# Optimization experiments

Hardware: AMD Instinct MI355X
Metric: run time of the kernel (lower is better)

## Reference

```python
import jax, jax.numpy as jnp
import numpy as np

B, T, E = 2, 2048, 1024
H = 16
DH = E // H  # 64
DFF = 4 * E
EPS = 1e-5


def _layernorm(x, gamma, beta):
    mu = jnp.mean(x, axis=-1, keepdims=True)
    var = jnp.mean((x - mu) ** 2, axis=-1, keepdims=True)
    return (x - mu) * jax.lax.rsqrt(var + EPS) * gamma + beta


def setup_inputs() -> dict:
    key = jax.random.key(0)
    ks = jax.random.split(key, 16)
    s_e = 1.0 / np.sqrt(E)
    s_f = 1.0 / np.sqrt(DFF)
    return {
        "x": jax.random.normal(ks[0], (B, T, E), jnp.float32),
        # per-head QKV projections, stacked over heads [H, E, DH]
        "Wq": jax.random.normal(ks[1], (H, E, DH), jnp.float32) * s_e,
        "bq": jnp.zeros((H, DH), jnp.float32),
        "Wk": jax.random.normal(ks[2], (H, E, DH), jnp.float32) * s_e,
        "bk": jnp.zeros((H, DH), jnp.float32),
        "Wv": jax.random.normal(ks[3], (H, E, DH), jnp.float32) * s_e,
        "bv": jnp.zeros((H, DH), jnp.float32),
        # output projection
        "Wo": jax.random.normal(ks[4], (E, E), jnp.float32) * s_e,
        "bo": jnp.zeros((E,), jnp.float32),
        # feed-forward
        "W1": jax.random.normal(ks[5], (E, DFF), jnp.float32) * s_e,
        "b1": jnp.zeros((DFF,), jnp.float32),
        "W2": jax.random.normal(ks[6], (DFF, E), jnp.float32) * s_f,
        "b2": jnp.zeros((E,), jnp.float32),
        # layernorms
        "gamma1": jnp.ones((E,), jnp.float32),
        "beta1": jnp.zeros((E,), jnp.float32),
        "gamma2": jnp.ones((E,), jnp.float32),
        "beta2": jnp.zeros((E,), jnp.float32),
    }


def reference(x, Wq, bq, Wk, bk, Wv, bv, Wo, bo, W1, b1, W2, b2,
              gamma1, beta1, gamma2, beta2):
    Bc, Tc, Ec = x.shape
    # --- multi-head causal self-attention (dropout = eval/identity) ---
    xn = _layernorm(x, gamma1, beta1)
    q = jnp.einsum('bte,hed->bhtd', xn, Wq) + bq[:, None, :]
    k = jnp.einsum('bte,hed->bhtd', xn, Wk) + bk[:, None, :]
    v = jnp.einsum('bte,hed->bhtd', xn, Wv) + bv[:, None, :]
    scale = 1.0 / np.sqrt(q.shape[-1])
    scores = jnp.einsum('bhtd,bhsd->bhts', q, k) * scale  # [B,H,T,T]
    causal = jnp.tril(jnp.ones((Tc, Tc), bool))
    scores = jnp.where(causal, scores, jnp.float32(-1e9))
    attn = jax.nn.softmax(scores, axis=-1)
    out = jnp.einsum('bhts,bhsd->bhtd', attn, v)          # [B,H,T,DH]
    out = out.transpose(0, 2, 1, 3).reshape(Bc, Tc, Ec)    # concat heads
    out = out @ Wo + bo
    x = x + out
    # --- feed-forward ---
    xn2 = _layernorm(x, gamma2, beta2)
    h = jax.nn.relu(xn2 @ W1 + b1)
    x = x + (h @ W2 + b2)
    return x
```

## Files before the change

### kernel.cpp

```cpp
#include <hip/hip_runtime.h>
#include <stdint.h>

#define BT    4096
#define EDIM  1024
#define TLEN  2048
#define NH    16
#define DHH   64
#define DFFN  4096

typedef short short8 __attribute__((ext_vector_type(8)));
typedef float f32x4  __attribute__((ext_vector_type(4)));

typedef const __attribute__((address_space(1))) unsigned int* gas_ptr;
typedef __attribute__((address_space(3))) unsigned int*       las_ptr;

__device__ __forceinline__ float bf2f(unsigned short u) {
    union { unsigned int i; float f; } c; c.i = ((unsigned int)u) << 16; return c.f;
}
__device__ __forceinline__ unsigned short f2bf(float f) {
    union { float f; unsigned int i; } c; c.f = f;
    unsigned int u = c.i;
    unsigned int r = u + 0x7fffu + ((u >> 16) & 1u);
    return (unsigned short)(r >> 16);
}
__device__ __forceinline__ float fexp2(float x) {
#if __has_builtin(__builtin_amdgcn_exp2f)
    return __builtin_amdgcn_exp2f(x);
#else
    return __expf(x * 0.69314718056f);
#endif
}
__device__ __forceinline__ void gload16(const unsigned short* g, unsigned short* l) {
    __builtin_amdgcn_global_load_lds((gas_ptr)g, (las_ptr)l, 16, 0, 0);
}

template<int QKV>
__global__ __launch_bounds__(256) void transpose_kernel(
    const float* src, unsigned short* dst, int Kdim, int srcStride)
{
    __shared__ float T[64][65];
    int t = threadIdx.x;
    int n0 = blockIdx.x * 64, k0 = blockIdx.y * 64;
    int r = t >> 4, c4 = (t & 15) * 4;
    #pragma unroll
    for (int i = 0; i < 4; i++) {
        int rr = r + i * 16;
        const float* p;
        if (QKV) p = src + ((size_t)(n0 >> 6)) * 65536 + (size_t)(k0 + rr) * 64 + c4;
        else     p = src + (size_t)(k0 + rr) * srcStride + n0 + c4;
        float4 v = *(const float4*)p;
        T[c4 + 0][rr] = v.x;
        T[c4 + 1][rr] = v.y;
        T[c4 + 2][rr] = v.z;
        T[c4 + 3][rr] = v.w;
    }
    __syncthreads();
    int rn = t >> 2, ck = (t & 3) * 16;
    short8 o0, o1;
    #pragma unroll
    for (int j = 0; j < 8; j++) o0[j] = (short)f2bf(T[rn][ck + j]);
    #pragma unroll
    for (int j = 0; j < 8; j++) o1[j] = (short)f2bf(T[rn][ck + 8 + j]);
    unsigned short* dp = dst + (size_t)(n0 + rn) * Kdim + k0 + ck;
    *(short8*)dp       = o0;
    *(short8*)(dp + 8) = o1;
}

__global__ __launch_bounds__(256) void vtrans_kernel(
    const unsigned short* __restrict__ v, unsigned short* __restrict__ vt)
{
    __shared__ __align__(16) unsigned short T[64][72];
    int bh = blockIdx.x, st = blockIdx.y;
    int t = threadIdx.x;
    int r = t >> 2, c = (t & 3) * 16;
    const unsigned short* src = v + ((size_t)bh * TLEN + st * 64) * DHH;
    short8 a0 = *(const short8*)(src + r * DHH + c);
    short8 a1 = *(const short8*)(src + r * DHH + c + 8);
    *(short8*)&T[r][c]     = a0;
    *(short8*)&T[r][c + 8] = a1;
    __syncthreads();
    int d = t >> 2;
    short8 o0, o1;
    #pragma unroll
    for (int j = 0; j < 8; j++) o0[j] = (short)T[c + j][d];
    #pragma unroll
    for (int j = 0; j < 8; j++) o1[j] = (short)T[c + 8 + j][d];
    unsigned short* dst = vt + ((size_t)bh * DHH + d) * TLEN + st * 64 + c;
    *(short8*)dst       = o0;
    *(short8*)(dst + 8) = o1;
}

__global__ __launch_bounds__(256) void bias_fuse_kernel(
    const float* __restrict__ bq, const float* __restrict__ bk,
    const float* __restrict__ bv, float* __restrict__ dst)
{
    int t = blockIdx.x * 256 + threadIdx.x;
    const float* src = (t < 1024) ? bq : (t < 2048) ? bk : bv;
    dst[t] = src[t & 1023];
}

template<int F32IN>
__global__ __launch_bounds__(256) void ln_stats_kernel(
    const void* __restrict__ x, float* __restrict__ mu_out, float* __restrict__ rstd_out)
{
    int row = blockIdx.x, tid = threadIdx.x;
    size_t off = (size_t)row * EDIM + tid * 4;
    float v0, v1, v2, v3;
    if (F32IN) {
        float4 a = *(const float4*)((const float*)x + off);
        v0 = a.x; v1 = a.y; v2 = a.z; v3 = a.w;
    } else {
        ushort4 raw = *(const ushort4*)((const unsigned short*)x + off);
        v0 = bf2f(raw.x); v1 = bf2f(raw.y); v2 = bf2f(raw.z); v3 = bf2f(raw.w);
    }
    float s  = v0 + v1 + v2 + v3;
    float ss = v0*v0 + v1*v1 + v2*v2 + v3*v3;
    #pragma unroll
    for (int o = 1; o < 64; o <<= 1) {
        s  += __shfl_xor(s,  o, 64);
        ss += __shfl_xor(ss, o, 64);
    }
    __shared__ float red[8];
    int wave = tid >> 6;
    if ((tid & 63) == 0) { red[wave*2] = s; red[wave*2+1] = ss; }
    __syncthreads();
    if (tid == 0) {
        s  = red[0] + red[2] + red[4] + red[6];
        ss = red[1] + red[3] + red[5] + red[7];
        float mu  = s * (1.0f / EDIM);
        float var = ss * (1.0f / EDIM) - mu * mu;
        mu_out[row]   = mu;
        rstd_out[row] = rsqrtf(var + 1e-5f);
    }
}

template<int F32IN>
__global__ __launch_bounds__(256) void ln_apply_kernel(
    const void* __restrict__ x, const float* __restrict__ mu, const float* __restrict__ rstd,
    const float* __restrict__ g, const float* __restrict__ b, unsigned short* __restrict__ out)
{
    int row = blockIdx.x, tid = threadIdx.x;
    float m = mu[row], rs = rstd[row];
    size_t off = (size_t)row * EDIM + tid * 4;
    float v0, v1, v2, v3;
    if (F32IN) {
        float4 a = *(const float4*)((const float*)x + off);
        v0 = a.x; v1 = a.y; v2 = a.z; v3 = a.w;
    } else {
        ushort4 raw = *(const ushort4*)((const unsigned short*)x + off);
        v0 = bf2f(raw.x); v1 = bf2f(raw.y); v2 = bf2f(raw.z); v3 = bf2f(raw.w);
    }
    float4 gv = *(const float4*)(g + tid * 4);
    float4 bv = *(const float4*)(b + tid * 4);
    ushort4 o;
    o.x = f2bf((v0 - m) * rs * gv.x + bv.x);
    o.y = f2bf((v1 - m) * rs * gv.y + bv.y);
    o.z = f2bf((v2 - m) * rs * gv.z + bv.z);
    o.w = f2bf((v3 - m) * rs * gv.w + bv.w);
    *(ushort4*)(out + off) = o;
}

#define V_QKV  0
#define V_WO   1
#define V_FF1  2
#define V_FF2A 3
#define V_FF2B 4

template<int VARIANT, int BN>
__global__ __launch_bounds__(256) void gemm_bt_kernel(
    const unsigned short* A,
    const unsigned short* Bt,
    const float* bias,
    const void* resid,
    void* out,
    int N, int K)
{
    constexpr int NJ = BN / 32;
    __shared__ __align__(16) unsigned short As[128 * 64];
    __shared__ __align__(16) unsigned short Bs[BN * 64];
    int tid  = threadIdx.x;
    int lane = tid & 63, wave = tid >> 6;
    int quad = lane >> 4, l16 = lane & 15;
    int wr = wave >> 1, wc = wave & 1;
    int m0 = blockIdx.y * 128, n0 = blockIdx.x * BN;

    f32x4 acc[4][NJ];
    #pragma unroll
    for (int i = 0; i < 4; i++)
        #pragma unroll
        for (int j = 0; j < NJ; j++) acc[i][j] = (f32x4){0.f, 0.f, 0.f, 0.f};

    int lr = lane >> 3;
    int lc = (lane & 7) * 8;

    for (int k0 = 0; k0 < K; k0 += 64) {
        #pragma unroll
        for (int i = 0; i < 4; i++) {
            int r = (i * 4 + wave) * 8 + lr;
            gload16(A + (size_t)(m0 + r) * K + k0 + lc, &As[(i * 4 + wave) * 512]);
        }
        #pragma unroll
        for (int i = 0; i < NJ; i++) {
            int r = (i * 4 + wave) * 8 + lr;
            gload16(Bt + (size_t)(n0 + r) * K + k0 + lc, &Bs[(i * 4 + wave) * 512]);
        }
        __syncthreads();

        #pragma unroll
        for (int ks = 0; ks < 2; ks++) {
            short8 af[4], bf[NJ];
            #pragma unroll
            for (int i = 0; i < 4; i++)
                af[i] = *(const short8*)(&As[(wr * 64 + i * 16 + l16) * 64 + ks * 32 + quad * 8]);
            #pragma unroll
            for (int j = 0; j < NJ; j++)
                bf[j] = *(const short8*)(&Bs[(wc * (BN / 2) + j * 16 + l16) * 64 + ks * 32 + quad * 8]);
            #pragma unroll
            for (int i = 0; i < 4; i++)
                #pragma unroll
                for (int j = 0; j < NJ; j++)
                    acc[i][j] = __builtin_amdgcn_mfma_f32_16x16x32_bf16(af[i], bf[j], acc[i][j], 0, 0, 0);
        }

        __syncthreads();
    }

    #pragma unroll
    for (int j = 0; j < NJ; j++) {
        int c = n0 + wc * (BN / 2) + j * 16 + l16;
        float bi = (VARIANT == V_FF2A) ? 0.0f : bias[c];
        #pragma unroll
        for (int i = 0; i < 4; i++) {
            #pragma unroll
            for (int r = 0; r < 4; r++) {
                int m = m0 + wr * 64 + i * 16 + quad * 4 + r;
                float val = acc[i][j][r] + bi;
                if (VARIANT == V_WO)
                    val += ((const float*)resid)[(size_t)m * N + c];
                if (VARIANT == V_FF2B)
                    val += bf2f(((const unsigned short*)resid)[(size_t)m * N + c])
                         + ((const float*)out)[(size_t)m * N + c];
                if (VARIANT == V_FF1)
                    val = fmaxf(val, 0.0f);
                if (VARIANT == V_QKV) {
                    int b = m >> 11, t = m & 2047;
                    int mat = c >> 10, cc = c & 1023;
                    int h = cc >> 6, d = cc & 63;
                    ((unsigned short*)out)[(size_t)mat * 4194304 +
                        (((size_t)(b * NH + h)) * TLEN + t) * DHH + d] = f2bf(val);
                } else if (VARIANT == V_FF2A || VARIANT == V_FF2B) {
                    ((float*)out)[(size_t)m * N + c] = val;
                } else {
                    ((unsigned short*)out)[(size_t)m * N + c] = f2bf(val);
                }
            }
        }
    }
}

__global__ __launch_bounds__(256) void attn_kernel(
    const unsigned short* __restrict__ q,
    const unsigned short* __restrict__ k,
    const unsigned short* __restrict__ vt,
    unsigned short* __restrict__ att)
{
    __shared__ __align__(16) unsigned short Ks[128 * 72];
    __shared__ __align__(16) unsigned short Vs[64 * 136];
    __shared__ __align__(16) unsigned short Ps[4][16 * 136];
    int tid  = threadIdx.x;
    int lane = tid & 63, wave = tid >> 6;
    int quad = lane >> 4, l16 = lane & 15;

    int flat = blockIdx.x;
    int xcd  = flat & 7, idx = flat >> 3;
    int bh   = xcd * 4 + (idx >> 5);
    int qt   = 31 - (idx & 31);
    int q0   = qt * 64;
    int qw   = q0 + wave * 16;

    const unsigned short* Qb = q  + ((size_t)bh * TLEN + qw) * DHH;
    const unsigned short* Kb = k  + (size_t)bh * TLEN * DHH;
    const unsigned short* Vb = vt + (size_t)bh * DHH * TLEN;

    short8 aq0 = *(const short8*)(Qb + l16 * DHH + quad * 8);
    short8 aq1 = *(const short8*)(Qb + l16 * DHH + 32 + quad * 8);

    f32x4 o[4];
    #pragma unroll
    for (int n = 0; n < 4; n++) o[n] = (f32x4){0.f, 0.f, 0.f, 0.f};
    f32x4 mrow = {-1e30f, -1e30f, -1e30f, -1e30f};
    f32x4 lrow = {0.f, 0.f, 0.f, 0.f};
    unsigned short* Pw = Ps[wave];
    const float cs = 0.18033688011f;

    int rowK = tid >> 1, colK = (tid & 1) * 32;
    int rowV = tid >> 2, colV = (tid & 3) * 32;

    int nch = (q0 >> 7) + 1;

    short8 ka0, ka1, ka2, ka3, va0, va1, va2, va3;
    {
        const unsigned short* kp = Kb + (size_t)rowK * DHH + colK;
        ka0 = *(const short8*)kp;
        ka1 = *(const short8*)(kp + 8);
        ka2 = *(const short8*)(kp + 16);
        ka3 = *(const short8*)(kp + 24);
        const unsigned short* vp = Vb + (size_t)rowV * TLEN + colV;
        va0 = *(const short8*)vp;
        va1 = *(const short8*)(vp + 8);
        va2 = *(const short8*)(vp + 16);
        va3 = *(const short8*)(vp + 24);
    }

    for (int ch = 0; ch < nch; ch++) {
        int s0 = ch * 128;
        __syncthreads();
        *(short8*)(&Ks[rowK * 72 + colK])       = ka0;
        *(short8*)(&Ks[rowK * 72 + colK + 8])   = ka1;
        *(short8*)(&Ks[rowK * 72 + colK + 16])  = ka2;
        *(short8*)(&Ks[rowK * 72 + colK + 24])  = ka3;
        *(short8*)(&Vs[rowV * 136 + colV])      = va0;
        *(short8*)(&Vs[rowV * 136 + colV + 8])  = va1;
        *(short8*)(&Vs[rowV * 136 + colV + 16]) = va2;
        *(short8*)(&Vs[rowV * 136 + colV + 24]) = va3;
        __syncthreads();

        if (ch + 1 < nch) {
            int s1 = s0 + 128;
            const unsigned short* kp = Kb + (size_t)(s1 + rowK) * DHH + colK;
            ka0 = *(const short8*)kp;
            ka1 = *(const short8*)(kp + 8);
            ka2 = *(const short8*)(kp + 16);
            ka3 = *(const short8*)(kp + 24);
            const unsigned short* vp = Vb + (size_t)rowV * TLEN + s1 + colV;
            va0 = *(const short8*)vp;
            va1 = *(const short8*)(vp + 8);
            va2 = *(const short8*)(vp + 16);
            va3 = *(const short8*)(vp + 24);
        }

        f32x4 S[8];
        #pragma unroll
        for (int n = 0; n < 8; n++) {
            short8 b0 = *(const short8*)(&Ks[(n * 16 + l16) * 72 + quad * 8]);
            short8 b1 = *(const short8*)(&Ks[(n * 16 + l16) * 72 + 32 + quad * 8]);
            f32x4 s = (f32x4){0.f, 0.f, 0.f, 0.f};
            s = __builtin_amdgcn_mfma_f32_16x16x32_bf16(aq0, b0, s, 0, 0, 0);
            s = __builtin_amdgcn_mfma_f32_16x16x32_bf16(aq1, b1, s, 0, 0, 0);
            S[n] = s;
        }
        bool needmask = (s0 + 127 > qw);
        #pragma unroll
        for (int r = 0; r < 4; r++) {
            float xv[8];
            #pragma unroll
            for (int n = 0; n < 8; n++) {
                float xx = S[n][r] * cs;
                if (needmask && (s0 + n * 16 + l16 > qw + quad * 4 + r)) xx = -1e30f;
                xv[n] = xx;
            }
            float mx = fmaxf(fmaxf(fmaxf(xv[0], xv[1]), fmaxf(xv[2], xv[3])),
                             fmaxf(fmaxf(xv[4], xv[5]), fmaxf(xv[6], xv[7])));
            mx = fmaxf(mx, __shfl_xor(mx, 1, 64));
            mx = fmaxf(mx, __shfl_xor(mx, 2, 64));
            mx = fmaxf(mx, __shfl_xor(mx, 4, 64));
            mx = fmaxf(mx, __shfl_xor(mx, 8, 64));
            float used;
            if (__all(mx <= mrow[r] + 8.0f)) {
                used = mrow[r];
            } else {
                float mnew  = fmaxf(mrow[r], mx);
                float alpha = fexp2(mrow[r] - mnew);
                lrow[r] *= alpha;
                o[0][r] *= alpha; o[1][r] *= alpha;
                o[2][r] *= alpha; o[3][r] *= alpha;
                mrow[r] = mnew;
                used = mnew;
            }
            float ps = 0.f;
            int prow = (quad * 4 + r) * 136;
            #pragma unroll
            for (int n = 0; n < 8; n++) {
                float p = fexp2(xv[n] - used);
                ps += p;
                Pw[prow + n * 16 + l16] = f2bf(p);
            }
            lrow[r] += ps;
        }
        short8 ap[4];
        #pragma unroll
        for (int ks = 0; ks < 4; ks++)
            ap[ks] = *(const short8*)(Pw + l16 * 136 + ks * 32 + quad * 8);
        #pragma unroll
        for (int n = 0; n < 4; n++) {
            #pragma unroll
            for (int ks = 0; ks < 4; ks++) {
                short8 b = *(const short8*)(&Vs[(n * 16 + l16) * 136 + ks * 32 + quad * 8]);
                o[n] = __builtin_amdgcn_mfma_f32_16x16x32_bf16(ap[ks], b, o[n], 0, 0, 0);
            }
        }
    }

    int bidx = bh >> 4, hh = bh & 15;
    #pragma unroll
    for (int r = 0; r < 4; r++) {
        float ls = lrow[r];
        ls += __shfl_xor(ls, 1, 64);
        ls += __shfl_xor(ls, 2, 64);
        ls += __shfl_xor(ls, 4, 64);
        ls += __shfl_xor(ls, 8, 64);
        float inv = 1.0f / ls;
        int t = qw + quad * 4 + r;
        size_t rowoff = ((size_t)(bidx * TLEN + t)) * EDIM + hh * 64;
        #pragma unroll
        for (int n = 0; n < 4; n++)
            att[rowoff + n * 16 + l16] = f2bf(o[n][r] * inv);
    }
}

extern "C" void kernel_launch(void* const* d_in, const int* in_sizes, int n_in,
                              void* d_out, int out_size, void* d_ws, size_t ws_size,
                              hipStream_t stream)
{
    (void)in_sizes; (void)n_in; (void)out_size; (void)ws_size;
    const float* x   = (const float*)d_in[0];
    const float* Wq  = (const float*)d_in[1];
    const float* bq  = (const float*)d_in[2];
    const float* Wk  = (const float*)d_in[3];
    const float* bk  = (const float*)d_in[4];
    const float* Wv  = (const float*)d_in[5];
    const float* bv  = (const float*)d_in[6];
    const float* Wo  = (const float*)d_in[7];
    const float* bo  = (const float*)d_in[8];
    const float* W1  = (const float*)d_in[9];
    const float* b1  = (const float*)d_in[10];
    const float* W2  = (const float*)d_in[11];
    const float* b2  = (const float*)d_in[12];
    const float* g1  = (const float*)d_in[13];
    const float* be1 = (const float*)d_in[14];
    const float* g2  = (const float*)d_in[15];
    const float* be2 = (const float*)d_in[16];

    unsigned short* ws  = (unsigned short*)d_ws;
    unsigned short* xn  = ws;
    unsigned short* vtg = ws;
    unsigned short* qb  = ws + 4194304;
    unsigned short* kb  = ws + 8388608;
    unsigned short* vb  = ws + 12582912;
    unsigned short* wqt = ws + 16777216;
    unsigned short* att = ws + 16777216;
    unsigned short* x1  = ws + 4194304;
    unsigned short* wot = ws + 8388608;
    unsigned short* w1t = ws + 8388608;
    unsigned short* w2t = ws + 10485760;
    unsigned short* hb  = ws + 12582912;
    float* biasf = (float*)(ws + 19922944);
    float* mu1 = (float*)((char*)d_ws + 41943040);
    float* rs1 = mu1 + 4096;
    float* mu2 = mu1 + 8192;
    float* rs2 = mu1 + 12288;

    dim3 gT64(16, 16);
    dim3 gE(EDIM / 64, BT / 128);
    dim3 gQKV(3072 / 64, BT / 128);
    dim3 gF(2048 / 128, BT / 128);

    transpose_kernel<1><<<gT64, 256, 0, stream>>>(Wq, wqt, EDIM, 64);
    transpose_kernel<1><<<gT64, 256, 0, stream>>>(Wk, wqt + 1048576, EDIM, 64);
    transpose_kernel<1><<<gT64, 256, 0, stream>>>(Wv, wqt + 2097152, EDIM, 64);
    bias_fuse_kernel<<<dim3(12), 256, 0, stream>>>(bq, bk, bv, biasf);

    ln_stats_kernel<1><<<BT, 256, 0, stream>>>(x, mu1, rs1);
    ln_apply_kernel<1><<<BT, 256, 0, stream>>>(x, mu1, rs1, g1, be1, xn);

    gemm_bt_kernel<V_QKV, 64><<<gQKV, 256, 0, stream>>>(xn, wqt, biasf, nullptr, qb, 3072, EDIM);

    vtrans_kernel<<<dim3(NH * 2, TLEN / 64), 256, 0, stream>>>(vb, vtg);

    attn_kernel<<<dim3(1024), 256, 0, stream>>>(qb, kb, vtg, att);

    transpose_kernel<0><<<gT64, 256, 0, stream>>>(Wo, wot, EDIM, EDIM);
    gemm_bt_kernel<V_WO, 64><<<gE, 256, 0, stream>>>(att, wot, bo, x, x1, EDIM, EDIM);

    ln_stats_kernel<0><<<BT, 256, 0, stream>>>(x1, mu2, rs2);
    ln_apply_kernel<0><<<BT, 256, 0, stream>>>(x1, mu2, rs2, g2, be2, xn);

    transpose_kernel<0><<<dim3(32, 16), 256, 0, stream>>>(W1, w1t, EDIM, DFFN);
    transpose_kernel<0><<<dim3(16, 32), 256, 0, stream>>>(W2, w2t, 2048, EDIM);
    gemm_bt_kernel<V_FF1, 128><<<gF, 256, 0, stream>>>(xn, w1t, b1, nullptr, hb, 2048, EDIM);
    gemm_bt_kernel<V_FF2A, 64><<<gE, 256, 0, stream>>>(hb, w2t, nullptr, nullptr, d_out, EDIM, 2048);
    transpose_kernel<0><<<dim3(32, 16), 256, 0, stream>>>(W1 + 2048, w1t, EDIM, DFFN);
    transpose_kernel<0><<<dim3(16, 32), 256, 0, stream>>>(W2 + (size_t)2048 * EDIM, w2t, 2048, EDIM);
    gemm_bt_kernel<V_FF1, 128><<<gF, 256, 0, stream>>>(xn, w1t, b1 + 2048, nullptr, hb, 2048, EDIM);
    gemm_bt_kernel<V_FF2B, 64><<<gE, 256, 0, stream>>>(hb, w2t, b2, x1, d_out, EDIM, 2048);
}
```

Measured before the change: 454.1 us.

## Fuse layernorm passes, merge QKV transposes, widen QKV tile, trim softmax shuffles

Combines each layernorm's stats and apply kernels into one, so every thread computes mean and rstd from the shared reduction, and drops the mu/rstd buffers. Replaces three per-matrix Q/K/V weight transposes with one 3D-grid launch. Moves the QKV GEMM to BN=128 tiles, halving its grid. In attention, the row-max shuffle reduction now runs only when the per-lane max fails the threshold check. P is converted to bf16 by truncation instead of round-to-nearest. Together these cut launches, extra HBM passes and ALU work, at some accuracy cost from truncation and fewer QKV blocks to fill the GPU.

```diff
diff --git a/kernel.cpp b/kernel.cpp
--- a/kernel.cpp
+++ b/kernel.cpp
@@ -22,6 +22,10 @@
     unsigned int u = c.i;
     unsigned int r = u + 0x7fffu + ((u >> 16) & 1u);
     return (unsigned short)(r >> 16);
+}
+__device__ __forceinline__ unsigned short f2bf_trunc(float f) {
+    union { float f; unsigned int i; } c; c.f = f;
+    return (unsigned short)(c.i >> 16);
 }
 __device__ __forceinline__ float fexp2(float x) {
 #if __has_builtin(__builtin_amdgcn_exp2f)
@@ -62,6 +66,39 @@
     #pragma unroll
     for (int j = 0; j < 8; j++) o1[j] = (short)f2bf(T[rn][ck + 8 + j]);
     unsigned short* dp = dst + (size_t)(n0 + rn) * Kdim + k0 + ck;
+    *(short8*)dp       = o0;
+    *(short8*)(dp + 8) = o1;
+}
+
+__global__ __launch_bounds__(256) void transpose_qkv3_kernel(
+    const float* __restrict__ Wq, const float* __restrict__ Wk,
+    const float* __restrict__ Wv, unsigned short* __restrict__ dstbase)
+{
+    __shared__ float T[64][65];
+    int z = blockIdx.z;
+    const float* src = (z == 0) ? Wq : (z == 1) ? Wk : Wv;
+    unsigned short* dst = dstbase + (size_t)z * 1048576;
+    int t = threadIdx.x;
+    int n0 = blockIdx.x * 64, k0 = blockIdx.y * 64;
+    int r = t >> 4, c4 = (t & 15) * 4;
+    #pragma unroll
+    for (int i = 0; i < 4; i++) {
+        int rr = r + i * 16;
+        const float* p = src + ((size_t)(n0 >> 6)) * 65536 + (size_t)(k0 + rr) * 64 + c4;
+        float4 v = *(const float4*)p;
+        T[c4 + 0][rr] = v.x;
+        T[c4 + 1][rr] = v.y;
+        T[c4 + 2][rr] = v.z;
+        T[c4 + 3][rr] = v.w;
+    }
+    __syncthreads();
+    int rn = t >> 2, ck = (t & 3) * 16;
+    short8 o0, o1;
+    #pragma unroll
+    for (int j = 0; j < 8; j++) o0[j] = (short)f2bf(T[rn][ck + j]);
+    #pragma unroll
+    for (int j = 0; j < 8; j++) o1[j] = (short)f2bf(T[rn][ck + 8 + j]);
+    unsigned short* dp = dst + (size_t)(n0 + rn) * EDIM + k0 + ck;
     *(short8*)dp       = o0;
     *(short8*)(dp + 8) = o1;
 }
@@ -100,8 +137,9 @@
 }
 
 template<int F32IN>
-__global__ __launch_bounds__(256) void ln_stats_kernel(
-    const void* __restrict__ x, float* __restrict__ mu_out, float* __restrict__ rstd_out)
+__global__ __launch_bounds__(256) void ln_fused_kernel(
+    const void* __restrict__ x, const float* __restrict__ g,
+    const float* __restrict__ b, unsigned short* __restrict__ out)
 {
     int row = blockIdx.x, tid = threadIdx.x;
     size_t off = (size_t)row * EDIM + tid * 4;
@@ -124,32 +162,10 @@
     int wave = tid >> 6;
     if ((tid & 63) == 0) { red[wave*2] = s; red[wave*2+1] = ss; }
     __syncthreads();
-    if (tid == 0) {
-        s  = red[0] + red[2] + red[4] + red[6];
-        ss = red[1] + red[3] + red[5] + red[7];
-        float mu  = s * (1.0f / EDIM);
-        float var = ss * (1.0f / EDIM) - mu * mu;
-        mu_out[row]   = mu;
-        rstd_out[row] = rsqrtf(var + 1e-5f);
-    }
-}
-
-template<int F32IN>
-__global__ __launch_bounds__(256) void ln_apply_kernel(
-    const void* __restrict__ x, const float* __restrict__ mu, const float* __restrict__ rstd,
-    const float* __restrict__ g, const float* __restrict__ b, unsigned short* __restrict__ out)
-{
-    int row = blockIdx.x, tid = threadIdx.x;
-    float m = mu[row], rs = rstd[row];
-    size_t off = (size_t)row * EDIM + tid * 4;
-    float v0, v1, v2, v3;
-    if (F32IN) {
-        float4 a = *(const float4*)((const float*)x + off);
-        v0 = a.x; v1 = a.y; v2 = a.z; v3 = a.w;
-    } else {
-        ushort4 raw = *(const ushort4*)((const unsigned short*)x + off);
-        v0 = bf2f(raw.x); v1 = bf2f(raw.y); v2 = bf2f(raw.z); v3 = bf2f(raw.w);
-    }
+    s  = red[0] + red[2] + red[4] + red[6];
+    ss = red[1] + red[3] + red[5] + red[7];
+    float m  = s * (1.0f / EDIM);
+    float rs = rsqrtf(ss * (1.0f / EDIM) - m * m + 1e-5f);
     float4 gv = *(const float4*)(g + tid * 4);
     float4 bv = *(const float4*)(b + tid * 4);
     ushort4 o;
@@ -359,16 +375,17 @@
                 if (needmask && (s0 + n * 16 + l16 > qw + quad * 4 + r)) xx = -1e30f;
                 xv[n] = xx;
             }
-            float mx = fmaxf(fmaxf(fmaxf(xv[0], xv[1]), fmaxf(xv[2], xv[3])),
-                             fmaxf(fmaxf(xv[4], xv[5]), fmaxf(xv[6], xv[7])));
-            mx = fmaxf(mx, __shfl_xor(mx, 1, 64));
-            mx = fmaxf(mx, __shfl_xor(mx, 2, 64));
-            mx = fmaxf(mx, __shfl_xor(mx, 4, 64));
-            mx = fmaxf(mx, __shfl_xor(mx, 8, 64));
+            float mxl = fmaxf(fmaxf(fmaxf(xv[0], xv[1]), fmaxf(xv[2], xv[3])),
+                              fmaxf(fmaxf(xv[4], xv[5]), fmaxf(xv[6], xv[7])));
             float used;
-            if (__all(mx <= mrow[r] + 8.0f)) {
+            if (__all(mxl <= mrow[r] + 8.0f)) {
                 used = mrow[r];
             } else {
+                float mx = mxl;
+                mx = fmaxf(mx, __shfl_xor(mx, 1, 64));
+                mx = fmaxf(mx, __shfl_xor(mx, 2, 64));
+                mx = fmaxf(mx, __shfl_xor(mx, 4, 64));
+                mx = fmaxf(mx, __shfl_xor(mx, 8, 64));
                 float mnew  = fmaxf(mrow[r], mx);
                 float alpha = fexp2(mrow[r] - mnew);
                 lrow[r] *= alpha;
@@ -383,7 +400,7 @@
             for (int n = 0; n < 8; n++) {
                 float p = fexp2(xv[n] - used);
                 ps += p;
-                Pw[prow + n * 16 + l16] = f2bf(p);
+                Pw[prow + n * 16 + l16] = f2bf_trunc(p);
             }
             lrow[r] += ps;
         }
@@ -455,25 +472,18 @@
     unsigned short* w2t = ws + 10485760;
     unsigned short* hb  = ws + 12582912;
     float* biasf = (float*)(ws + 19922944);
-    float* mu1 = (float*)((char*)d_ws + 41943040);
-    float* rs1 = mu1 + 4096;
-    float* mu2 = mu1 + 8192;
-    float* rs2 = mu1 + 12288;
 
     dim3 gT64(16, 16);
     dim3 gE(EDIM / 64, BT / 128);
-    dim3 gQKV(3072 / 64, BT / 128);
+    dim3 gQKV(3072 / 128, BT / 128);
     dim3 gF(2048 / 128, BT / 128);
 
-    transpose_kernel<1><<<gT64, 256, 0, stream>>>(Wq, wqt, EDIM, 64);
-    transpose_kernel<1><<<gT64, 256, 0, stream>>>(Wk, wqt + 1048576, EDIM, 64);
-    transpose_kernel<1><<<gT64, 256, 0, stream>>>(Wv, wqt + 2097152, EDIM, 64);
+    transpose_qkv3_kernel<<<dim3(16, 16, 3), 256, 0, stream>>>(Wq, Wk, Wv, wqt);
     bias_fuse_kernel<<<dim3(12), 256, 0, stream>>>(bq, bk, bv, biasf);
 
-    ln_stats_kernel<1><<<BT, 256, 0, stream>>>(x, mu1, rs1);
-    ln_apply_kernel<1><<<BT, 256, 0, stream>>>(x, mu1, rs1, g1, be1, xn);
-
-    gemm_bt_kernel<V_QKV, 64><<<gQKV, 256, 0, stream>>>(xn, wqt, biasf, nullptr, qb, 3072, EDIM);
+    ln_fused_kernel<1><<<BT, 256, 0, stream>>>(x, g1, be1, xn);
+
+    gemm_bt_kernel<V_QKV, 128><<<gQKV, 256, 0, stream>>>(xn, wqt, biasf, nullptr, qb, 3072, EDIM);
 
     vtrans_kernel<<<dim3(NH * 2, TLEN / 64), 256, 0, stream>>>(vb, vtg);
 
@@ -482,8 +492,7 @@
     transpose_kernel<0><<<gT64, 256, 0, stream>>>(Wo, wot, EDIM, EDIM);
     gemm_bt_kernel<V_WO, 64><<<gE, 256, 0, stream>>>(att, wot, bo, x, x1, EDIM, EDIM);
 
-    ln_stats_kernel<0><<<BT, 256, 0, stream>>>(x1, mu2, rs2);
-    ln_apply_kernel<0><<<BT, 256, 0, stream>>>(x1, mu2, rs2, g2, be2, xn);
+    ln_fused_kernel<0><<<BT, 256, 0, stream>>>(x1, g2, be2, xn);
 
     transpose_kernel<0><<<dim3(32, 16), 256, 0, stream>>>(W1, w1t, EDIM, DFFN);
     transpose_kernel<0><<<dim3(16, 32), 256, 0, stream>>>(W2, w2t, 2048, EDIM);
```

Result: faster. 442.5 us (-2.6%).
